# Kernel optimization log

Hardware: AMD Instinct MI355X
Metric: run time of the kernel (lower is better)

The kernel has to match this reference:

```python
import jax, jax.numpy as jnp
import numpy as np

N, D = 8192, 256
NEG_BIG = -9e15


def setup_inputs() -> dict:
    key = jax.random.key(0)
    k1, k2, k3 = jax.random.split(key, 3)
    h = jax.random.normal(k1, (N, D), dtype=jnp.float32)
    adj = jax.random.randint(k2, (N, N), 0, 2, dtype=jnp.int32)
    # xavier_uniform for a of shape (2D, 1): bound = sqrt(6/(2D+1))
    bound = np.sqrt(6.0 / (2 * D + 1)).astype(np.float32)
    a = jax.random.uniform(k3, (2 * D, 1), dtype=jnp.float32, minval=-bound, maxval=bound)
    return {"h": h, "adj": adj, "a": a}


def reference(h, adj, a):
    d = h.shape[1]
    h1 = h @ a[:d]            # [N, 1]
    h2 = h @ a[d:]            # [N, 1]
    e = jax.nn.leaky_relu(h1 + h2.T, negative_slope=0.01)  # [N, N]
    attention = jnp.where(adj > 0, e, NEG_BIG)
    attention = jax.nn.softmax(attention, axis=1)
    # dropout skipped: eval mode (training=False)
    return attention @ h      # [N, D]
```

## Files before the change

kernel.cpp:

```cpp
#include <hip/hip_runtime.h>
#include <hip/hip_bf16.h>

#define NTOT 8192
#define DDIM 256
#define RT 32
#define JSPLIT 8
#define JCHUNK (NTOT / JSPLIT)
#define NBODY (JCHUNK / 16)
#define JBSTR 520

typedef __attribute__((ext_vector_type(8)))  short short8;
typedef __attribute__((ext_vector_type(16))) float floatx16;

__global__ __launch_bounds__(256) void gat_scores(const float* __restrict__ h,
                                                  const float* __restrict__ a,
                                                  float4* __restrict__ rc,
                                                  float2* __restrict__ etab) {
  int row  = blockIdx.x * 4 + (threadIdx.x >> 6);
  int lane = threadIdx.x & 63;
  const float* hr = h + (size_t)row * DDIM;
  float p1 = 0.f, p2 = 0.f;
#pragma unroll
  for (int k = 0; k < DDIM / 64; ++k) {
    int idx  = lane + 64 * k;
    float hv = hr[idx];
    p1 += hv * a[idx];
    p2 += hv * a[DDIM + idx];
  }
#pragma unroll
  for (int off = 32; off > 0; off >>= 1) {
    p1 += __shfl_down(p1, off, 64);
    p2 += __shfl_down(p2, off, 64);
  }
  if (lane == 0) {
    rc[row]   = make_float4(__expf(p1), __expf(0.01f * p1), __expf(-p1), 0.f);
    etab[row] = make_float2(__expf(p2), __expf(0.01f * p2));
  }
}

__global__ __launch_bounds__(256) void gat_hpack(const float* __restrict__ h,
                                                 ushort* __restrict__ hTf2) {
  __shared__ float tile[64][257];
  const int t    = threadIdx.x;
  const int lane = t & 63;
  const int w    = t >> 6;
  const int half = lane >> 5;
  const int l31  = lane & 31;
  const int j0   = blockIdx.x * 64;

#pragma unroll
  for (int it = 0; it < 16; ++it) {
    int r = it * 4 + w;
    float4 v = *(const float4*)(h + (size_t)(j0 + r) * DDIM + lane * 4);
    tile[r][lane * 4 + 0] = v.x; tile[r][lane * 4 + 1] = v.y;
    tile[r][lane * 4 + 2] = v.z; tile[r][lane * 4 + 3] = v.w;
  }
  __syncthreads();

  const int jb = blockIdx.x * 4 + w;
#pragma unroll
  for (int nb = 0; nb < 8; ++nb) {
    short8 vv;
#pragma unroll
    for (int i = 0; i < 8; ++i) {
      float f = tile[w * 16 + half * 8 + i][nb * 32 + l31];
      __hip_bfloat16 b = __float2bfloat16(f);
      vv[i] = *(short*)&b;
    }
    *(short8*)(hTf2 + ((size_t)nb * JBSTR + jb) * 512 + lane * 8) = vv;
  }
}

__global__ __launch_bounds__(256, 2) void gat_attn(const ushort* __restrict__ hTf2,
                                                   const int*   __restrict__ adj,
                                                   const float4* __restrict__ rc,
                                                   const float* __restrict__ etabf,
                                                   float* __restrict__ part,
                                                   float* __restrict__ lpart) {
  const int t    = threadIdx.x;
  const int lane = t & 63;
  const int w    = t >> 6;
  const int half = lane >> 5;
  const int l31  = lane & 31;
  const int wg   = blockIdx.x * 4 + w;
  const int rtile = wg & 255;
  const int js    = wg >> 8;
  const int rbase = rtile * RT;
  const int jbase = js * JCHUNK;
  const int row   = rbase + l31;

  const float4 rcv = rc[row];
  const float E1 = rcv.x, E2 = rcv.y, T = rcv.z;

  const int*    adjp = adj + (size_t)row * NTOT + jbase + half * 8;
  const float*  etp  = etabf + 2 * (jbase + half * 8);
  const ushort* bfp  = hTf2 + (size_t)(js * 64) * 512 + lane * 8;

  floatx16 acc[8];
#pragma unroll
  for (int nb = 0; nb < 8; ++nb)
#pragma unroll
    for (int r = 0; r < 16; ++r) acc[nb][r] = 0.f;
  float lp = 0.f;

  int4   aR[2][2];
  float4 eR[2][4];
#pragma unroll
  for (int p = 0; p < 2; ++p) {
    aR[p][0] = ((const int4*)(adjp + p * 16))[0];
    aR[p][1] = ((const int4*)(adjp + p * 16 + 4))[0];
    eR[p][0] = ((const float4*)(etp + p * 32))[0];
    eR[p][1] = ((const float4*)(etp + p * 32 + 4))[0];
    eR[p][2] = ((const float4*)(etp + p * 32 + 8))[0];
    eR[p][3] = ((const float4*)(etp + p * 32 + 12))[0];
  }

#define BODY(jt, P)                                                            \
  {                                                                            \
             \
    short8 bfr[8];                                                             \
    const ushort* bp = bfp + (size_t)(jt) * 512;                               \
    _Pragma("unroll")                                                          \
    for (int nb = 0; nb < 8; ++nb)                                             \
      bfr[nb] = *(const short8*)(bp + (size_t)nb * (JBSTR * 512));             \
                                                \
    const int* am = (const int*)aR[P];                                         \
    short8 pa;                                                                 \
    _Pragma("unroll")                                                          \
    for (int i = 0; i < 8; ++i) {                                              \
      const float t1 = eR[P][i >> 1][(i & 1) ? 2 : 0];                         \
      const float t2 = eR[P][i >> 1][(i & 1) ? 3 : 1];                         \
      float v = (t1 > T) ? E1 * t1 : E2 * t2;                                  \
      v = (am[i] > 0) ? v : 0.f;                                               \
      lp += v;                                                                 \
      __hip_bfloat16 b = __float2bfloat16(v);                                  \
      pa[i] = *(short*)&b;                                                     \
    }                                                                          \
                                   \
    if ((jt) + 2 < NBODY) {                                                    \
      aR[P][0] = ((const int4*)(adjp + ((jt) + 2) * 16))[0];                   \
      aR[P][1] = ((const int4*)(adjp + ((jt) + 2) * 16 + 4))[0];               \
      const float* en = etp + ((jt) + 2) * 32;                                 \
      eR[P][0] = ((const float4*)(en))[0];                                     \
      eR[P][1] = ((const float4*)(en + 4))[0];                                 \
      eR[P][2] = ((const float4*)(en + 8))[0];                                 \
      eR[P][3] = ((const float4*)(en + 12))[0];                                \
    }                                                                          \
    _Pragma("unroll")                                                          \
    for (int nb = 0; nb < 8; ++nb)                                             \
      acc[nb] = __builtin_amdgcn_mfma_f32_32x32x16_bf16(pa, bfr[nb],           \
                                                        acc[nb], 0, 0, 0);     \
  }

  for (int jt = 0; jt < NBODY; jt += 2) {
    BODY(jt, 0)
    BODY(jt + 1, 1)
  }
#undef BODY

  lp += __shfl_xor(lp, 32, 64);
  if (lane < 32) lpart[(size_t)js * NTOT + rbase + lane] = lp;

  float* pp = part + ((size_t)js * NTOT + rbase) * DDIM;
#pragma unroll
  for (int nb = 0; nb < 8; ++nb)
#pragma unroll
    for (int reg = 0; reg < 16; ++reg) {
      int rloc = (reg & 3) + 8 * (reg >> 2) + 4 * half;
      pp[(size_t)rloc * DDIM + nb * 32 + l31] = acc[nb][reg];
    }
}

__global__ __launch_bounds__(256) void gat_reduce(const float* __restrict__ part,
                                                  const float* __restrict__ lpart,
                                                  float* __restrict__ out) {
  const int row = blockIdx.x;
  const int t   = threadIdx.x;
  float l = 0.f;
#pragma unroll
  for (int js = 0; js < JSPLIT; ++js) l += lpart[(size_t)js * NTOT + row];
  float s = 0.f;
#pragma unroll
  for (int js = 0; js < JSPLIT; ++js)
    s += part[((size_t)js * NTOT + row) * DDIM + t];
  out[(size_t)row * DDIM + t] = s / l;
}

extern "C" void kernel_launch(void* const* d_in, const int* in_sizes, int n_in,
                              void* d_out, int out_size, void* d_ws, size_t ws_size,
                              hipStream_t stream) {
  const float* h   = (const float*)d_in[0];
  const int*   adj = (const int*)d_in[1];
  const float* a   = (const float*)d_in[2];
  float* out = (float*)d_out;
  char* ws = (char*)d_ws;

  float4* rc    = (float4*)(ws);
  float2* etab  = (float2*)(ws + (256 << 10));
  ushort* hTf2  = (ushort*)(ws + (1 << 20));
  float*  part  = (float*)(ws + (8 << 20));
  float*  lpart = (float*)(ws + (80 << 20));

  gat_scores<<<NTOT / 4, 256, 0, stream>>>(h, a, rc, etab);
  gat_hpack<<<NTOT / 64, 256, 0, stream>>>(h, hTf2);
  gat_attn<<<512, 256, 0, stream>>>(hTf2, adj, rc, (const float*)etab, part, lpart);
  gat_reduce<<<NTOT, 256, 0, stream>>>(part, lpart, out);
}
```

Baseline: 511.9 us.

## Pack adjacency into transposed bitmask and retile attention waves over rows and columns

Adds a pre-pass that converts the int32 adjacency matrix into a transposed bitmask, so the attention kernel reads 1 bit per edge instead of 4 bytes. The attention kernel is retiled so each wave handles 128 rows by 64 output columns rather than 32 rows by all 256 columns. This cuts per-wave B-fragment loads and the register pressure of holding eight B fragments. The full adjacency still has to be read once in the pack pass. Probability values are now recomputed for each of the 4 column groups, which adds exp/select work in exchange for fewer memory loads.

Measured after the change: 650.0 us. +27.0%, slower.

```diff
diff --git a/kernel.cpp b/kernel.cpp
--- a/kernel.cpp
+++ b/kernel.cpp
@@ -3,7 +3,6 @@
 
 #define NTOT 8192
 #define DDIM 256
-#define RT 32
 #define JSPLIT 8
 #define JCHUNK (NTOT / JSPLIT)
 #define NBODY (JCHUNK / 16)
@@ -35,6 +34,39 @@
   if (lane == 0) {
     rc[row]   = make_float4(__expf(p1), __expf(0.01f * p1), __expf(-p1), 0.f);
     etab[row] = make_float2(__expf(p2), __expf(0.01f * p2));
+  }
+}
+
+__global__ __launch_bounds__(256) void gat_pack(const int* __restrict__ adj,
+                                                unsigned* __restrict__ bitsT) {
+  __shared__ unsigned words[64][65];
+  const int t    = threadIdx.x;
+  const int lane = t & 63;
+  const int w    = t >> 6;
+  const int r0   = blockIdx.x * 64;
+  const int jb   = blockIdx.y * 2048;
+
+#pragma unroll 2
+  for (int rr = 0; rr < 16; ++rr) {
+    const int rl = w * 16 + rr;
+    const int* ap = adj + (size_t)(r0 + rl) * NTOT + jb + lane * 4;
+#pragma unroll
+    for (int R = 0; R < 8; ++R) {
+      int4 v = *(const int4*)(ap + R * 256);
+      unsigned nib = (v.x > 0 ? 1u : 0u) | (v.y > 0 ? 2u : 0u) |
+                     (v.z > 0 ? 4u : 0u) | (v.w > 0 ? 8u : 0u);
+      unsigned b8  = nib | (__shfl_xor((int)nib, 1, 64) << 4);
+      unsigned b16 = b8  | (__shfl_xor((int)b8,  2, 64) << 8);
+      unsigned b32 = b16 | (__shfl_xor((int)b16, 4, 64) << 16);
+      if ((lane & 7) == 0) words[rl][R * 8 + (lane >> 3)] = b32;
+    }
+  }
+  __syncthreads();
+
+#pragma unroll 4
+  for (int kk = 0; kk < 16; ++kk) {
+    const int jwl = w * 16 + kk;
+    bitsT[(size_t)(jb / 32 + jwl) * NTOT + r0 + lane] = words[lane][jwl];
   }
 }
 
@@ -72,7 +104,7 @@
 }
 
 __global__ __launch_bounds__(256, 2) void gat_attn(const ushort* __restrict__ hTf2,
-                                                   const int*   __restrict__ adj,
+                                                   const unsigned* __restrict__ bitsT,
                                                    const float4* __restrict__ rc,
                                                    const float* __restrict__ etabf,
                                                    float* __restrict__ part,
@@ -83,92 +115,115 @@
   const int half = lane >> 5;
   const int l31  = lane & 31;
   const int wg   = blockIdx.x * 4 + w;
-  const int rtile = wg & 255;
-  const int js    = wg >> 8;
-  const int rbase = rtile * RT;
+  const int js   = wg & 7;
+  const int cg   = (wg >> 3) & 3;
+  const int rg   = wg >> 5;
+  const int rbase = rg * 128;
   const int jbase = js * JCHUNK;
-  const int row   = rbase + l31;
-
-  const float4 rcv = rc[row];
-  const float E1 = rcv.x, E2 = rcv.y, T = rcv.z;
-
-  const int*    adjp = adj + (size_t)row * NTOT + jbase + half * 8;
-  const float*  etp  = etabf + 2 * (jbase + half * 8);
-  const ushort* bfp  = hTf2 + (size_t)(js * 64) * 512 + lane * 8;
-
-  floatx16 acc[8];
-#pragma unroll
-  for (int nb = 0; nb < 8; ++nb)
-#pragma unroll
-    for (int r = 0; r < 16; ++r) acc[nb][r] = 0.f;
-  float lp = 0.f;
-
-  int4   aR[2][2];
+  const int jb32  = jbase / 32;
+  const int jb16  = jbase / 16;
+
+  float E1[4], E2[4], Tt[4];
+#pragma unroll
+  for (int t4 = 0; t4 < 4; ++t4) {
+    float4 v = rc[rbase + 32 * t4 + l31];
+    E1[t4] = v.x; E2[t4] = v.y; Tt[t4] = v.z;
+  }
+
+  const unsigned* btp = bitsT + (size_t)jb32 * NTOT + rbase + l31;
+  const float*    etp = etabf + 2 * (jbase + half * 8);
+  const ushort*   bfp = hTf2 + ((size_t)(2 * cg) * JBSTR + jb16) * 512 + lane * 8;
+
+  floatx16 acc[4][2];
+#pragma unroll
+  for (int t4 = 0; t4 < 4; ++t4)
+#pragma unroll
+    for (int q = 0; q < 2; ++q)
+#pragma unroll
+      for (int r = 0; r < 16; ++r) acc[t4][q][r] = 0.f;
+  float lp[4] = {0.f, 0.f, 0.f, 0.f};
+
   float4 eR[2][4];
-#pragma unroll
-  for (int p = 0; p < 2; ++p) {
-    aR[p][0] = ((const int4*)(adjp + p * 16))[0];
-    aR[p][1] = ((const int4*)(adjp + p * 16 + 4))[0];
-    eR[p][0] = ((const float4*)(etp + p * 32))[0];
-    eR[p][1] = ((const float4*)(etp + p * 32 + 4))[0];
-    eR[p][2] = ((const float4*)(etp + p * 32 + 8))[0];
-    eR[p][3] = ((const float4*)(etp + p * 32 + 12))[0];
-  }
-
-#define BODY(jt, P)                                                            \
+  short8 bR[2][2];
+#pragma unroll
+  for (int P = 0; P < 2; ++P) {
+#pragma unroll
+    for (int k = 0; k < 4; ++k)
+      eR[P][k] = ((const float4*)(etp + P * 32))[k];
+#pragma unroll
+    for (int q = 0; q < 2; ++q)
+      bR[P][q] = *(const short8*)(bfp + ((size_t)q * JBSTR + P) * 512);
+  }
+  unsigned W[4];
+#pragma unroll
+  for (int t4 = 0; t4 < 4; ++t4) W[t4] = btp[32 * t4];
+
+#define BODY(JT, P, P16)                                                       \
   {                                                                            \
-             \
-    short8 bfr[8];                                                             \
-    const ushort* bp = bfp + (size_t)(jt) * 512;                               \
+    short8 pa[4];                                                              \
     _Pragma("unroll")                                                          \
-    for (int nb = 0; nb < 8; ++nb)                                             \
-      bfr[nb] = *(const short8*)(bp + (size_t)nb * (JBSTR * 512));             \
-                                                \
-    const int* am = (const int*)aR[P];                                         \
-    short8 pa;                                                                 \
-    _Pragma("unroll")                                                          \
-    for (int i = 0; i < 8; ++i) {                                              \
-      const float t1 = eR[P][i >> 1][(i & 1) ? 2 : 0];                         \
-      const float t2 = eR[P][i >> 1][(i & 1) ? 3 : 1];                         \
-      float v = (t1 > T) ? E1 * t1 : E2 * t2;                                  \
-      v = (am[i] > 0) ? v : 0.f;                                               \
-      lp += v;                                                                 \
-      __hip_bfloat16 b = __float2bfloat16(v);                                  \
-      pa[i] = *(short*)&b;                                                     \
+    for (int t4 = 0; t4 < 4; ++t4) {                                           \
+      const unsigned bm = (W[t4] >> ((P16) + half * 8)) & 0xffu;               \
+      _Pragma("unroll")                                                        \
+      for (int i = 0; i < 8; ++i) {                                            \
+        const float t1v = eR[P][i >> 1][(i & 1) ? 2 : 0];                      \
+        const float t2v = eR[P][i >> 1][(i & 1) ? 3 : 1];                      \
+        float v = (t1v > Tt[t4]) ? E1[t4] * t1v : E2[t4] * t2v;                \
+        v = ((bm >> i) & 1u) ? v : 0.f;                                        \
+        lp[t4] += v;                                                           \
+        __hip_bfloat16 b = __float2bfloat16(v);                                \
+        pa[t4][i] = *(short*)&b;                                               \
+      }                                                                        \
     }                                                                          \
-                                   \
-    if ((jt) + 2 < NBODY) {                                                    \
-      aR[P][0] = ((const int4*)(adjp + ((jt) + 2) * 16))[0];                   \
-      aR[P][1] = ((const int4*)(adjp + ((jt) + 2) * 16 + 4))[0];               \
-      const float* en = etp + ((jt) + 2) * 32;                                 \
-      eR[P][0] = ((const float4*)(en))[0];                                     \
-      eR[P][1] = ((const float4*)(en + 4))[0];                                 \
-      eR[P][2] = ((const float4*)(en + 8))[0];                                 \
-      eR[P][3] = ((const float4*)(en + 12))[0];                                \
+    short8 b0 = bR[P][0], b1 = bR[P][1];                                       \
+    if ((JT) + 2 < NBODY) {                                                    \
+      const float* en = etp + ((JT) + 2) * 32;                                 \
+      _Pragma("unroll")                                                        \
+      for (int k = 0; k < 4; ++k) eR[P][k] = ((const float4*)en)[k];           \
+      _Pragma("unroll")                                                        \
+      for (int q = 0; q < 2; ++q)                                              \
+        bR[P][q] = *(const short8*)(bfp + ((size_t)q * JBSTR + (JT) + 2) * 512); \
     }                                                                          \
     _Pragma("unroll")                                                          \
-    for (int nb = 0; nb < 8; ++nb)                                             \
-      acc[nb] = __builtin_amdgcn_mfma_f32_32x32x16_bf16(pa, bfr[nb],           \
-                                                        acc[nb], 0, 0, 0);     \
-  }
-
-  for (int jt = 0; jt < NBODY; jt += 2) {
-    BODY(jt, 0)
-    BODY(jt + 1, 1)
+    for (int t4 = 0; t4 < 4; ++t4) {                                           \
+      acc[t4][0] = __builtin_amdgcn_mfma_f32_32x32x16_bf16(pa[t4], b0, acc[t4][0], 0, 0, 0); \
+      acc[t4][1] = __builtin_amdgcn_mfma_f32_32x32x16_bf16(pa[t4], b1, acc[t4][1], 0, 0, 0); \
+    }                                                                          \
+  }
+
+  for (int g = 0; g < 32; ++g) {
+    unsigned Wn[4];
+    if (g + 1 < 32) {
+#pragma unroll
+      for (int t4 = 0; t4 < 4; ++t4)
+        Wn[t4] = btp[(size_t)(g + 1) * NTOT + 32 * t4];
+    }
+    const int jt = 2 * g;
+    BODY(jt, 0, 0)
+    BODY(jt + 1, 1, 16)
+#pragma unroll
+    for (int t4 = 0; t4 < 4; ++t4) W[t4] = Wn[t4];
   }
 #undef BODY
 
-  lp += __shfl_xor(lp, 32, 64);
-  if (lane < 32) lpart[(size_t)js * NTOT + rbase + lane] = lp;
-
-  float* pp = part + ((size_t)js * NTOT + rbase) * DDIM;
-#pragma unroll
-  for (int nb = 0; nb < 8; ++nb)
-#pragma unroll
-    for (int reg = 0; reg < 16; ++reg) {
-      int rloc = (reg & 3) + 8 * (reg >> 2) + 4 * half;
-      pp[(size_t)rloc * DDIM + nb * 32 + l31] = acc[nb][reg];
-    }
+#pragma unroll
+  for (int t4 = 0; t4 < 4; ++t4) lp[t4] += __shfl_xor(lp[t4], 32, 64);
+  if (cg == 0 && lane < 32) {
+#pragma unroll
+    for (int t4 = 0; t4 < 4; ++t4)
+      lpart[(size_t)js * NTOT + rbase + 32 * t4 + lane] = lp[t4];
+  }
+
+  float* pp = part + ((size_t)js * NTOT + rbase) * DDIM + cg * 64;
+#pragma unroll
+  for (int t4 = 0; t4 < 4; ++t4)
+#pragma unroll
+    for (int q = 0; q < 2; ++q)
+#pragma unroll
+      for (int reg = 0; reg < 16; ++reg) {
+        int rloc = (reg & 3) + 8 * (reg >> 2) + 4 * half;
+        pp[(size_t)(32 * t4 + rloc) * DDIM + q * 32 + l31] = acc[t4][q][reg];
+      }
 }
 
 __global__ __launch_bounds__(256) void gat_reduce(const float* __restrict__ part,
@@ -195,14 +250,16 @@
   float* out = (float*)d_out;
   char* ws = (char*)d_ws;
 
-  float4* rc    = (float4*)(ws);
-  float2* etab  = (float2*)(ws + (256 << 10));
-  ushort* hTf2  = (ushort*)(ws + (1 << 20));
-  float*  part  = (float*)(ws + (8 << 20));
-  float*  lpart = (float*)(ws + (80 << 20));
+  float4*   rc    = (float4*)(ws);
+  float2*   etab  = (float2*)(ws + (256 << 10));
+  unsigned* bitsT = (unsigned*)(ws + (1 << 20));
+  ushort*   hTf2  = (ushort*)(ws + (10 << 20));
+  float*    part  = (float*)(ws + (16 << 20));
+  float*    lpart = (float*)(ws + (82 << 20));
 
   gat_scores<<<NTOT / 4, 256, 0, stream>>>(h, a, rc, etab);
+  gat_pack<<<dim3(NTOT / 64, 4), 256, 0, stream>>>(adj, bitsT);
   gat_hpack<<<NTOT / 64, 256, 0, stream>>>(h, hTf2);
-  gat_attn<<<512, 256, 0, stream>>>(hTf2, adj, rc, (const float*)etab, part, lpart);
+  gat_attn<<<512, 256, 0, stream>>>(hTf2, bitsT, rc, (const float*)etab, part, lpart);
   gat_reduce<<<NTOT, 256, 0, stream>>>(part, lpart, out);
 }
```

## Share attention tile via LDS across eight waves splitting output columns

Applied to the files above, without the earlier changes.

The attention kernel is restructured into 512-thread blocks of 32 rows. All threads cooperatively compute the masked exponentiated scores for a 128-column chunk and stage them in double-buffered shared memory. Each of the eight waves then multiplies that shared tile against its own 32-column slice of the bf16 h, instead of one wave owning all 256 output columns. The key split drops from 8 to 4, adjacency loads become contiguous 128-int row segments, and the precomputed exponential factorization is replaced by a per-element leaky_relu plus __expf. The aim is lower accumulator register pressure, higher occupancy and better coalescing, at the cost of a block barrier per chunk and more transcendental work.

Result: faster. 469.5 us (-8.3%).

```diff
diff --git a/kernel.cpp b/kernel.cpp
--- a/kernel.cpp
+++ b/kernel.cpp
@@ -3,10 +3,10 @@
 
 #define NTOT 8192
 #define DDIM 256
-#define RT 32
-#define JSPLIT 8
+#define JSPLIT 4
 #define JCHUNK (NTOT / JSPLIT)
-#define NBODY (JCHUNK / 16)
+#define BK 128
+#define NCHUNK (JCHUNK / BK)
 #define JBSTR 520
 
 typedef __attribute__((ext_vector_type(8)))  short short8;
@@ -14,8 +14,8 @@
 
 __global__ __launch_bounds__(256) void gat_scores(const float* __restrict__ h,
                                                   const float* __restrict__ a,
-                                                  float4* __restrict__ rc,
-                                                  float2* __restrict__ etab) {
+                                                  float* __restrict__ s1,
+                                                  float* __restrict__ s2) {
   int row  = blockIdx.x * 4 + (threadIdx.x >> 6);
   int lane = threadIdx.x & 63;
   const float* hr = h + (size_t)row * DDIM;
@@ -32,10 +32,7 @@
     p1 += __shfl_down(p1, off, 64);
     p2 += __shfl_down(p2, off, 64);
   }
-  if (lane == 0) {
-    rc[row]   = make_float4(__expf(p1), __expf(0.01f * p1), __expf(-p1), 0.f);
-    etab[row] = make_float2(__expf(p2), __expf(0.01f * p2));
-  }
+  if (lane == 0) { s1[row] = p1; s2[row] = p2; }
 }
 
 __global__ __launch_bounds__(256) void gat_hpack(const float* __restrict__ h,
@@ -71,104 +68,107 @@
   }
 }
 
-__global__ __launch_bounds__(256, 2) void gat_attn(const ushort* __restrict__ hTf2,
+__global__ __launch_bounds__(512, 4) void gat_attn(const ushort* __restrict__ hTf2,
                                                    const int*   __restrict__ adj,
-                                                   const float4* __restrict__ rc,
-                                                   const float* __restrict__ etabf,
+                                                   const float* __restrict__ s1g,
+                                                   const float* __restrict__ s2g,
                                                    float* __restrict__ part,
                                                    float* __restrict__ lpart) {
+  __shared__ ushort pbuf[2][16 * 33 * 8];
+  __shared__ float  lred[32][17];
+
   const int t    = threadIdx.x;
   const int lane = t & 63;
   const int w    = t >> 6;
   const int half = lane >> 5;
   const int l31  = lane & 31;
-  const int wg   = blockIdx.x * 4 + w;
-  const int rtile = wg & 255;
-  const int js    = wg >> 8;
-  const int rbase = rtile * RT;
+  const int bx   = blockIdx.x;
+  const int slot = bx & 7;
+  const int js   = slot >> 1;
+  const int rg   = (bx >> 3) * 2 + (slot & 1);
+  const int r0   = rg * 32;
   const int jbase = js * JCHUNK;
-  const int row   = rbase + l31;
-
-  const float4 rcv = rc[row];
-  const float E1 = rcv.x, E2 = rcv.y, T = rcv.z;
-
-  const int*    adjp = adj + (size_t)row * NTOT + jbase + half * 8;
-  const float*  etp  = etabf + 2 * (jbase + half * 8);
-  const ushort* bfp  = hTf2 + (size_t)(js * 64) * 512 + lane * 8;
-
-  floatx16 acc[8];
-#pragma unroll
-  for (int nb = 0; nb < 8; ++nb)
-#pragma unroll
-    for (int r = 0; r < 16; ++r) acc[nb][r] = 0.f;
+
+  const int pr  = t >> 4;
+  const int seg = t & 15;
+  const int prow = r0 + pr;
+  const float s1v = s1g[prow];
+
+  const int*   adjp = adj + (size_t)prow * NTOT + jbase + seg * 8;
+  const float* s2p  = s2g + jbase + seg * 8;
+  const ushort* bfp = hTf2 + ((size_t)w * JBSTR + jbase / 16) * 512 + lane * 8;
+
+  floatx16 acc;
+#pragma unroll
+  for (int r = 0; r < 16; ++r) acc[r] = 0.f;
   float lp = 0.f;
 
-  int4   aR[2][2];
-  float4 eR[2][4];
-#pragma unroll
-  for (int p = 0; p < 2; ++p) {
-    aR[p][0] = ((const int4*)(adjp + p * 16))[0];
-    aR[p][1] = ((const int4*)(adjp + p * 16 + 4))[0];
-    eR[p][0] = ((const float4*)(etp + p * 32))[0];
-    eR[p][1] = ((const float4*)(etp + p * 32 + 4))[0];
-    eR[p][2] = ((const float4*)(etp + p * 32 + 8))[0];
-    eR[p][3] = ((const float4*)(etp + p * 32 + 12))[0];
-  }
-
-#define BODY(jt, P)                                                            \
-  {                                                                            \
-             \
-    short8 bfr[8];                                                             \
-    const ushort* bp = bfp + (size_t)(jt) * 512;                               \
-    _Pragma("unroll")                                                          \
-    for (int nb = 0; nb < 8; ++nb)                                             \
-      bfr[nb] = *(const short8*)(bp + (size_t)nb * (JBSTR * 512));             \
-                                                \
-    const int* am = (const int*)aR[P];                                         \
-    short8 pa;                                                                 \
-    _Pragma("unroll")                                                          \
-    for (int i = 0; i < 8; ++i) {                                              \
-      const float t1 = eR[P][i >> 1][(i & 1) ? 2 : 0];                         \
-      const float t2 = eR[P][i >> 1][(i & 1) ? 3 : 1];                         \
-      float v = (t1 > T) ? E1 * t1 : E2 * t2;                                  \
-      v = (am[i] > 0) ? v : 0.f;                                               \
-      lp += v;                                                                 \
-      __hip_bfloat16 b = __float2bfloat16(v);                                  \
-      pa[i] = *(short*)&b;                                                     \
-    }                                                                          \
-                                   \
-    if ((jt) + 2 < NBODY) {                                                    \
-      aR[P][0] = ((const int4*)(adjp + ((jt) + 2) * 16))[0];                   \
-      aR[P][1] = ((const int4*)(adjp + ((jt) + 2) * 16 + 4))[0];               \
-      const float* en = etp + ((jt) + 2) * 32;                                 \
-      eR[P][0] = ((const float4*)(en))[0];                                     \
-      eR[P][1] = ((const float4*)(en + 4))[0];                                 \
-      eR[P][2] = ((const float4*)(en + 8))[0];                                 \
-      eR[P][3] = ((const float4*)(en + 12))[0];                                \
-    }                                                                          \
-    _Pragma("unroll")                                                          \
-    for (int nb = 0; nb < 8; ++nb)                                             \
-      acc[nb] = __builtin_amdgcn_mfma_f32_32x32x16_bf16(pa, bfr[nb],           \
-                                                        acc[nb], 0, 0, 0);     \
-  }
-
-  for (int jt = 0; jt < NBODY; jt += 2) {
-    BODY(jt, 0)
-    BODY(jt + 1, 1)
+  int4   a0A = ((const int4*)adjp)[0],        a0B = ((const int4*)(adjp + 4))[0];
+  int4   a1A = ((const int4*)(adjp + BK))[0], a1B = ((const int4*)(adjp + BK + 4))[0];
+  float4 s0A = ((const float4*)s2p)[0],        s0B = ((const float4*)(s2p + 4))[0];
+  float4 s1A = ((const float4*)(s2p + BK))[0], s1B = ((const float4*)(s2p + BK + 4))[0];
+
+#define PK(i, mi, sv)                                                    \
+  {                                                                      \
+    float e = s1v + (sv);                                                \
+    e = fmaxf(e, 0.01f * e);                                             \
+    float p = ((mi) > 0) ? __expf(e) : 0.f;                              \
+    lp += p;                                                             \
+    __hip_bfloat16 b = __float2bfloat16(p);                              \
+    pw[i] = *(short*)&b;                                                 \
+  }
+
+#define BODY(C, AA, AB, SA, SB, PAR)                                     \
+  {                                                                      \
+     \
+    short8 bfr[8];                                                       \
+    _Pragma("unroll")                                                    \
+    for (int kc = 0; kc < 8; ++kc)                                       \
+      bfr[kc] = *(const short8*)(bfp + (size_t)((C) * 8 + kc) * 512);    \
+                            \
+    short8 pw;                                                           \
+    PK(0, AA.x, SA.x) PK(1, AA.y, SA.y) PK(2, AA.z, SA.z) PK(3, AA.w, SA.w) \
+    PK(4, AB.x, SB.x) PK(5, AB.y, SB.y) PK(6, AB.z, SB.z) PK(7, AB.w, SB.w) \
+    *(short8*)&pbuf[PAR][(seg * 33 + pr) * 8] = pw;                      \
+                                          \
+    if ((C) + 2 < NCHUNK) {                                              \
+      AA = ((const int4*)(adjp + ((C) + 2) * BK))[0];                    \
+      AB = ((const int4*)(adjp + ((C) + 2) * BK + 4))[0];                \
+      SA = ((const float4*)(s2p + ((C) + 2) * BK))[0];                   \
+      SB = ((const float4*)(s2p + ((C) + 2) * BK + 4))[0];               \
+    }                                                                    \
+    __syncthreads();     \
+                          \
+    _Pragma("unroll")                                                    \
+    for (int kc = 0; kc < 8; ++kc) {                                     \
+      const int jg = kc * 2 + half;                                      \
+      short8 af = *(const short8*)&pbuf[PAR][(jg * 33 + l31) * 8];       \
+      acc = __builtin_amdgcn_mfma_f32_32x32x16_bf16(af, bfr[kc], acc, 0, 0, 0); \
+    }                                                                    \
+  }
+
+  for (int c = 0; c < NCHUNK; c += 2) {
+    BODY(c,     a0A, a0B, s0A, s0B, 0)
+    BODY(c + 1, a1A, a1B, s1A, s1B, 1)
   }
 #undef BODY
-
-  lp += __shfl_xor(lp, 32, 64);
-  if (lane < 32) lpart[(size_t)js * NTOT + rbase + lane] = lp;
-
-  float* pp = part + ((size_t)js * NTOT + rbase) * DDIM;
-#pragma unroll
-  for (int nb = 0; nb < 8; ++nb)
-#pragma unroll
-    for (int reg = 0; reg < 16; ++reg) {
-      int rloc = (reg & 3) + 8 * (reg >> 2) + 4 * half;
-      pp[(size_t)rloc * DDIM + nb * 32 + l31] = acc[nb][reg];
-    }
+#undef PK
+
+  lred[pr][seg] = lp;
+  __syncthreads();
+  if (t < 32) {
+    float s = 0.f;
+#pragma unroll
+    for (int k = 0; k < 16; ++k) s += lred[t][k];
+    lpart[(size_t)js * NTOT + r0 + t] = s;
+  }
+
+  float* pp = part + ((size_t)js * NTOT + r0) * DDIM + w * 32 + l31;
+#pragma unroll
+  for (int reg = 0; reg < 16; ++reg) {
+    const int rloc = (reg & 3) + 8 * (reg >> 2) + 4 * half;
+    pp[(size_t)rloc * DDIM] = acc[reg];
+  }
 }
 
 __global__ __launch_bounds__(256) void gat_reduce(const float* __restrict__ part,
@@ -195,14 +195,14 @@
   float* out = (float*)d_out;
   char* ws = (char*)d_ws;
 
-  float4* rc    = (float4*)(ws);
-  float2* etab  = (float2*)(ws + (256 << 10));
+  float*  s1    = (float*)(ws);
+  float*  s2    = (float*)(ws + (64 << 10));
   ushort* hTf2  = (ushort*)(ws + (1 << 20));
   float*  part  = (float*)(ws + (8 << 20));
-  float*  lpart = (float*)(ws + (80 << 20));
-
-  gat_scores<<<NTOT / 4, 256, 0, stream>>>(h, a, rc, etab);
+  float*  lpart = (float*)(ws + (48 << 20));
+
+  gat_scores<<<NTOT / 4, 256, 0, stream>>>(h, a, s1, s2);
   gat_hpack<<<NTOT / 64, 256, 0, stream>>>(h, hTf2);
-  gat_attn<<<512, 256, 0, stream>>>(hTf2, adj, rc, (const float*)etab, part, lpart);
+  gat_attn<<<1024, 512, 0, stream>>>(hTf2, adj, s1, s2, part, lpart);
   gat_reduce<<<NTOT, 256, 0, stream>>>(part, lpart, out);
 }
```
